# Kernel tuning notes

Measured on AMD Instinct MI355X. Metric: run time of the kernel, lower is better.

The kernel has to match this reference:

```python
import jax, jax.numpy as jnp
import numpy as np

D_MODEL = 1024
N_HEADS = 16
D_HEAD = D_MODEL // N_HEADS
SPARSE_THRESH = 0.09
MASK_FILL = -1e9


def setup_inputs() -> dict:
    key = jax.random.key(0)
    ks = jax.random.split(key, 11)
    B, S, D = 4, 1024, D_MODEL
    # Xavier-uniform bound for square [D, D] linear weights
    bound = float(np.sqrt(6.0 / (D + D)))

    def xavier(k):
        return jax.random.uniform(k, (D, D), jnp.float32, -bound, bound)

    return {
        "q": jax.random.normal(ks[0], (B, S, D), jnp.float32),
        "k": jax.random.normal(ks[1], (B, S, D), jnp.float32),
        "v": jax.random.normal(ks[2], (B, S, D), jnp.float32),
        "Wq": xavier(ks[3]), "bq": jnp.zeros((D,), jnp.float32),
        "Wk": xavier(ks[4]), "bk": jnp.zeros((D,), jnp.float32),
        "Wv": xavier(ks[5]), "bv": jnp.zeros((D,), jnp.float32),
        "Wo": xavier(ks[6]), "bo": jnp.zeros((D,), jnp.float32),
    }


def reference(q, k, v, Wq, bq, Wk, bk, Wv, bv, Wo, bo):
    B, S, D = q.shape
    H, dk = N_HEADS, D_HEAD

    def proj(x, W, b):
        # nn.Linear: x @ W^T + b, then split heads -> [B, H, S, dk]
        y = jnp.einsum("bsd,ed->bse", x, W) + b
        return y.reshape(B, S, H, dk).transpose(0, 2, 1, 3)

    qh = proj(q, Wq, bq)
    kh = proj(k, Wk, bk)
    vh = proj(v, Wv, bv)

    scale = 1.0 / jnp.sqrt(jnp.asarray(dk, q.dtype))
    scores = jnp.einsum("bhqd,bhkd->bhqk", qh, kh) * scale  # [B,H,S,S]

    att1 = jax.nn.softmax(scores, axis=-1)
    # mask entries whose first-pass probability is below the sparsity threshold
    scores2 = jnp.where(att1 < SPARSE_THRESH, jnp.asarray(MASK_FILL, scores.dtype), scores)
    att2 = jax.nn.softmax(scores2, axis=-1)
    # dropout(p=0.2) is identity in eval mode (deterministic reference)

    ctx = jnp.einsum("bhqk,bhkd->bhqd", att2, vh)           # [B,H,S,dk]
    ctx = ctx.transpose(0, 2, 1, 3).reshape(B, S, D)
    return jnp.einsum("bsd,ed->bse", ctx, Wo) + bo
```

## Files before the change

kernel.cpp:

```cpp
#include <hip/hip_runtime.h>
#include <hip/hip_bf16.h>
#include <math.h>


constexpr int D_MODEL = 1024;
constexpr int N_HEADS = 16;
constexpr int D_HEAD  = 64;
constexpr int SEQ     = 1024;
constexpr int BATCH   = 4;
constexpr float SPARSE_THRESH = 0.09f;

typedef short  bf16x8 __attribute__((ext_vector_type(8)));
typedef float  f32x4  __attribute__((ext_vector_type(4)));

__device__ __forceinline__ unsigned short f2bf_rne(float x) {
    unsigned u = __float_as_uint(x);
    u += 0x7FFFu + ((u >> 16) & 1u);
    return (unsigned short)(u >> 16);
}
__device__ __forceinline__ float bf2f(unsigned short b) {
    return __uint_as_float(((unsigned)b) << 16);
}

__device__ __forceinline__ unsigned cvt2(float a, float b) {
    __hip_bfloat162 p = __float22bfloat162_rn(make_float2(a, b));
    unsigned u; __builtin_memcpy(&u, &p, 4); return u;
}
__device__ __forceinline__ void split4(float x0, float x1, float x2, float x3,
                                       unsigned* hw, unsigned* lw) {
    const unsigned uh0 = cvt2(x0, x1);
    hw[0] = uh0;
    lw[0] = cvt2(x0 - __uint_as_float(uh0 << 16),
                 x1 - __uint_as_float(uh0 & 0xFFFF0000u));
    const unsigned uh1 = cvt2(x2, x3);
    hw[1] = uh1;
    lw[1] = cvt2(x2 - __uint_as_float(uh1 << 16),
                 x3 - __uint_as_float(uh1 & 0xFFFF0000u));
}

union BF8 { unsigned u[4]; bf16x8 v; };

__device__ __forceinline__ void unpack_pair(const unsigned* u, bf16x8& hi, bf16x8& lo) {
    BF8 h, l;
    #pragma unroll
    for (int p = 0; p < 4; ++p) {
        h.u[p] = (u[2 * p] >> 16)      | (u[2 * p + 1] & 0xFFFF0000u);
        l.u[p] = (u[2 * p] & 0xFFFFu)  | (u[2 * p + 1] << 16);
    }
    hi = h.v; lo = l.v;
}

__global__ __launch_bounds__(256)
void conv_w(const float* __restrict__ Wq, const float* __restrict__ Wk,
            const float* __restrict__ Wv,
            unsigned short* __restrict__ Wqh, unsigned short* __restrict__ Wql,
            unsigned short* __restrict__ Wkh, unsigned short* __restrict__ Wkl,
            unsigned short* __restrict__ Wvh, unsigned short* __restrict__ Wvl)
{
    const int NW8 = (D_MODEL * D_MODEL) / 8;
    int i = blockIdx.x * 256 + threadIdx.x;
    const float* s; unsigned short *dh, *dl;
    if (i < NW8)            { s = Wq; dh = Wqh; dl = Wql; }
    else if (i < 2 * NW8)   { i -= NW8; s = Wk; dh = Wkh; dl = Wkl; }
    else                    { i -= 2 * NW8; s = Wv; dh = Wvh; dl = Wvl; }
    const float4 x0 = ((const float4*)(s + (size_t)i * 8))[0];
    const float4 x1 = ((const float4*)(s + (size_t)i * 8))[1];
    unsigned hw[4], lw[4];
    split4(x0.x, x0.y, x0.z, x0.w, &hw[0], &lw[0]);
    split4(x1.x, x1.y, x1.z, x1.w, &hw[2], &lw[2]);
    *(uint4*)&dh[(size_t)i * 8] = *(const uint4*)hw;
    *(uint4*)&dl[(size_t)i * 8] = *(const uint4*)lw;
}

__global__ __launch_bounds__(256, 3)
void proj_qkv(const float* __restrict__ q, const float* __restrict__ k,
              const float* __restrict__ v,
              const unsigned short* __restrict__ Wqh, const unsigned short* __restrict__ Wql,
              const unsigned short* __restrict__ Wkh, const unsigned short* __restrict__ Wkl,
              const unsigned short* __restrict__ Wvh, const unsigned short* __restrict__ Wvl,
              const float* __restrict__ bq, const float* __restrict__ bk,
              const float* __restrict__ bv,
              unsigned* __restrict__ qp, unsigned* __restrict__ kp,
              unsigned short* __restrict__ vt)
{
    __shared__ unsigned short SM[4][128][40];
    unsigned short (*A_h)[40] = SM[0];
    unsigned short (*A_l)[40] = SM[1];
    unsigned short (*B_h)[40] = SM[2];
    unsigned short (*B_l)[40] = SM[3];

    const int z = blockIdx.z;
    const float* X    = (z == 0) ? q   : (z == 1) ? k   : v;
    const unsigned short* Wh = (z == 0) ? Wqh : (z == 1) ? Wkh : Wvh;
    const unsigned short* Wl = (z == 0) ? Wql : (z == 1) ? Wkl : Wvl;
    const float* bias = (z == 0) ? bq  : (z == 1) ? bk  : bv;
    const float scale = (z == 0) ? 0.125f : 1.0f;

    const int K = D_MODEL;
    const int tid = threadIdx.x, lane = tid & 63;
    const int l15 = lane & 15, l4 = lane >> 4;
    const int wv4 = tid >> 6;
    const int wr = (wv4 >> 1) * 64, wc = (wv4 & 1) * 64;
    const int bm = blockIdx.x * 128, bn = blockIdx.y * 128;
    const int sr = tid >> 1, sh = (tid & 1) * 16;

    f32x4 acc[4][4];
    #pragma unroll
    for (int i = 0; i < 4; ++i)
        #pragma unroll
        for (int j = 0; j < 4; ++j) acc[i][j] = (f32x4){0.f, 0.f, 0.f, 0.f};

    const float* ga = X + (size_t)(bm + sr) * K + sh;
    const unsigned short* gbh = Wh + (size_t)(bn + sr) * K + sh;
    const unsigned short* gbl = Wl + (size_t)(bn + sr) * K + sh;

    float4 av[4];
    uint4 wbh0, wbh1, wbl0, wbl1;
    #pragma unroll
    for (int l = 0; l < 4; ++l) av[l] = *(const float4*)&ga[l * 4];
    wbh0 = *(const uint4*)&gbh[0]; wbh1 = *(const uint4*)&gbh[8];
    wbl0 = *(const uint4*)&gbl[0]; wbl1 = *(const uint4*)&gbl[8];

    #pragma unroll 1
    for (int k0 = 0; k0 < K; k0 += 32) {
        unsigned ahw[8], alw[8];
        #pragma unroll
        for (int l = 0; l < 4; ++l)
            split4(av[l].x, av[l].y, av[l].z, av[l].w, &ahw[l * 2], &alw[l * 2]);

        __syncthreads();
        *(uint4*)&A_h[sr][sh]     = *(const uint4*)&ahw[0];
        *(uint4*)&A_h[sr][sh + 8] = *(const uint4*)&ahw[4];
        *(uint4*)&A_l[sr][sh]     = *(const uint4*)&alw[0];
        *(uint4*)&A_l[sr][sh + 8] = *(const uint4*)&alw[4];
        *(uint4*)&B_h[sr][sh]     = wbh0;
        *(uint4*)&B_h[sr][sh + 8] = wbh1;
        *(uint4*)&B_l[sr][sh]     = wbl0;
        *(uint4*)&B_l[sr][sh + 8] = wbl1;
        __syncthreads();

        if (k0 + 32 < K) {
            const int o = k0 + 32;
            #pragma unroll
            for (int l = 0; l < 4; ++l) av[l] = *(const float4*)&ga[o + l * 4];
            wbh0 = *(const uint4*)&gbh[o]; wbh1 = *(const uint4*)&gbh[o + 8];
            wbl0 = *(const uint4*)&gbl[o]; wbl1 = *(const uint4*)&gbl[o + 8];
        }

        bf16x8 ah[4], al4[4], bh4[4], bl4[4];
        #pragma unroll
        for (int i = 0; i < 4; ++i) {
            const int r = wr + i * 16 + l15;
            const int c = wc + i * 16 + l15;
            ah[i]  = *(const bf16x8*)&A_h[r][l4 * 8];
            al4[i] = *(const bf16x8*)&A_l[r][l4 * 8];
            bh4[i] = *(const bf16x8*)&B_h[c][l4 * 8];
            bl4[i] = *(const bf16x8*)&B_l[c][l4 * 8];
        }
        #pragma unroll
        for (int i = 0; i < 4; ++i)
            #pragma unroll
            for (int j = 0; j < 4; ++j) {
                acc[i][j] = __builtin_amdgcn_mfma_f32_16x16x32_bf16(ah[i],  bh4[j], acc[i][j], 0, 0, 0);
                acc[i][j] = __builtin_amdgcn_mfma_f32_16x16x32_bf16(ah[i],  bl4[j], acc[i][j], 0, 0, 0);
                acc[i][j] = __builtin_amdgcn_mfma_f32_16x16x32_bf16(al4[i], bh4[j], acc[i][j], 0, 0, 0);
            }
    }

    if (z == 2) {
        unsigned short* T = &SM[0][0][0];
        __syncthreads();
        #pragma unroll
        for (int i = 0; i < 4; ++i)
            #pragma unroll
            for (int j = 0; j < 4; ++j) {
                const int cl = wc + j * 16 + l15;
                const int sl = wr + i * 16 + l4 * 4;
                const float bi = bias[bn + cl];
                unsigned short h4[4];
                #pragma unroll
                for (int r = 0; r < 4; ++r)
                    h4[r] = f2bf_rne(acc[i][j][r] + bi);
                *(uint2*)&T[cl * 136 + sl] = *(const uint2*)&h4[0];
            }
        __syncthreads();
        const int c = tid >> 1, half = tid & 1;
        const int bb = bm >> 10;
        const int sb = (bm & (SEQ - 1)) + half * 64;
        unsigned short* dst = vt + (((size_t)bb << 20) + (size_t)(bn + c) * SEQ + sb);
        const unsigned short* srcT = &T[c * 136 + half * 64];
        #pragma unroll
        for (int u = 0; u < 8; ++u)
            *(uint4*)&dst[u * 8] = *(const uint4*)&srcT[u * 8];
        return;
    }

    unsigned* Cp = (z == 0) ? qp : kp;
    #pragma unroll
    for (int i = 0; i < 4; ++i)
        #pragma unroll
        for (int j = 0; j < 4; ++j) {
            const int rb = bm + wr + i * 16 + l4 * 4;
            const int c  = bn + wc + j * 16 + l15;
            const float bi = bias[c];
            const int h = c >> 6, d = c & (D_HEAD - 1);
            #pragma unroll
            for (int r = 0; r < 4; ++r) {
                const float val = (acc[i][j][r] + bi) * scale;
                const unsigned short hu = f2bf_rne(val);
                const unsigned short lu = f2bf_rne(val - bf2f(hu));
                const int mrow = rb + r;
                const int b = mrow >> 10, s = mrow & (SEQ - 1);
                Cp[((size_t)(b * N_HEADS + h) * SEQ + s) * D_HEAD + d] =
                    ((unsigned)hu << 16) | lu;
            }
        }
}

__global__ __launch_bounds__(256, 3)
void proj_o(const unsigned short* __restrict__ Act, const float* __restrict__ W,
            const float* __restrict__ bias, float* __restrict__ out)
{
    __shared__ unsigned short A_h[128][40];
    __shared__ unsigned short B_h[128][40];

    const int K = D_MODEL;
    const int tid = threadIdx.x, lane = tid & 63;
    const int l15 = lane & 15, l4 = lane >> 4;
    const int wv4 = tid >> 6;
    const int wr = (wv4 >> 1) * 64, wc = (wv4 & 1) * 64;
    const int bm = blockIdx.x * 128, bn = blockIdx.y * 128;
    const int sr = tid >> 1, sh = (tid & 1) * 16;

    f32x4 acc[4][4];
    #pragma unroll
    for (int i = 0; i < 4; ++i)
        #pragma unroll
        for (int j = 0; j < 4; ++j) acc[i][j] = (f32x4){0.f, 0.f, 0.f, 0.f};

    const unsigned short* ga = Act + (size_t)(bm + sr) * K + sh;
    const float* gb = W + (size_t)(bn + sr) * K + sh;

    uint4 av0 = *(const uint4*)&ga[0], av1 = *(const uint4*)&ga[8];
    float4 bv4[4];
    #pragma unroll
    for (int l = 0; l < 4; ++l) bv4[l] = *(const float4*)&gb[l * 4];

    #pragma unroll 1
    for (int k0 = 0; k0 < K; k0 += 32) {
        unsigned bhw[8];
        #pragma unroll
        for (int l = 0; l < 4; ++l) {
            bhw[l * 2]     = cvt2(bv4[l].x, bv4[l].y);
            bhw[l * 2 + 1] = cvt2(bv4[l].z, bv4[l].w);
        }

        __syncthreads();
        *(uint4*)&A_h[sr][sh]     = av0;
        *(uint4*)&A_h[sr][sh + 8] = av1;
        *(uint4*)&B_h[sr][sh]     = *(const uint4*)&bhw[0];
        *(uint4*)&B_h[sr][sh + 8] = *(const uint4*)&bhw[4];
        __syncthreads();

        if (k0 + 32 < K) {
            av0 = *(const uint4*)&ga[k0 + 32];
            av1 = *(const uint4*)&ga[k0 + 32 + 8];
            #pragma unroll
            for (int l = 0; l < 4; ++l)
                bv4[l] = *(const float4*)&gb[k0 + 32 + l * 4];
        }

        bf16x8 ah[4], bh4[4];
        #pragma unroll
        for (int i = 0; i < 4; ++i) {
            ah[i]  = *(const bf16x8*)&A_h[wr + i * 16 + l15][l4 * 8];
            bh4[i] = *(const bf16x8*)&B_h[wc + i * 16 + l15][l4 * 8];
        }
        #pragma unroll
        for (int i = 0; i < 4; ++i)
            #pragma unroll
            for (int j = 0; j < 4; ++j)
                acc[i][j] = __builtin_amdgcn_mfma_f32_16x16x32_bf16(ah[i], bh4[j], acc[i][j], 0, 0, 0);
    }

    #pragma unroll
    for (int i = 0; i < 4; ++i)
        #pragma unroll
        for (int j = 0; j < 4; ++j) {
            const int rb = bm + wr + i * 16 + l4 * 4;
            const int c  = bn + wc + j * 16 + l15;
            const float bi = bias[c];
            #pragma unroll
            for (int r = 0; r < 4; ++r)
                out[(size_t)(rb + r) * D_MODEL + c] = acc[i][j][r] + bi;
        }
}

__device__ __forceinline__ void score_from_lds(
    const unsigned short (* __restrict__ KH)[72], const unsigned short (* __restrict__ KL)[72],
    int l15, int l4, const bf16x8 (&qh)[2][2], const bf16x8 (&ql)[2][2], f32x4 acc[2][4])
{
    #pragma unroll
    for (int j = 0; j < 4; ++j) {
        const int row = l15 + 16 * j;
        const bf16x8 kh0 = *(const bf16x8*)&KH[row][l4 * 8];
        const bf16x8 kh1 = *(const bf16x8*)&KH[row][32 + l4 * 8];
        const bf16x8 kl0 = *(const bf16x8*)&KL[row][l4 * 8];
        const bf16x8 kl1 = *(const bf16x8*)&KL[row][32 + l4 * 8];
        #pragma unroll
        for (int st = 0; st < 2; ++st) {
            f32x4 a = (f32x4){0.f, 0.f, 0.f, 0.f};
            a = __builtin_amdgcn_mfma_f32_16x16x32_bf16(qh[st][0], kh0, a, 0, 0, 0);
            a = __builtin_amdgcn_mfma_f32_16x16x32_bf16(qh[st][0], kl0, a, 0, 0, 0);
            a = __builtin_amdgcn_mfma_f32_16x16x32_bf16(ql[st][0], kh0, a, 0, 0, 0);
            a = __builtin_amdgcn_mfma_f32_16x16x32_bf16(qh[st][1], kh1, a, 0, 0, 0);
            a = __builtin_amdgcn_mfma_f32_16x16x32_bf16(qh[st][1], kl1, a, 0, 0, 0);
            a = __builtin_amdgcn_mfma_f32_16x16x32_bf16(ql[st][1], kh1, a, 0, 0, 0);
            acc[st][j] = a;
        }
    }
}

__global__ __launch_bounds__(256, 3)
void attn_mfma(const unsigned* __restrict__ qp, const unsigned* __restrict__ kp,
               const unsigned short* __restrict__ vt, unsigned short* __restrict__ ctxh)
{
    __shared__ unsigned short KHL[2][2][64][72];
    __shared__ unsigned short Wl[4][32][64];
    __shared__ float Vm[64];
    __shared__ int AnyNU;
    float (*Pm)[4] = (float (*)[4])&Wl[0][0][0];

    const int tid  = threadIdx.x;
    const int lane = tid & 63;
    const int wv   = tid >> 6;
    const int l15  = lane & 15, l4 = lane >> 4;
    const int bh   = blockIdx.x;
    const int b    = bh >> 4, h = bh & 15;
    const int q0   = blockIdx.y * 128 + wv * 32;

    bf16x8 qh[2][2], ql[2][2];
    #pragma unroll
    for (int st = 0; st < 2; ++st) {
        const unsigned* qrow = qp + ((size_t)bh * SEQ + q0 + st * 16 + l15) * D_HEAD;
        #pragma unroll
        for (int ks = 0; ks < 2; ++ks) {
            unsigned u[8];
            *(uint4*)&u[0] = *(const uint4*)&qrow[ks * 32 + l4 * 8];
            *(uint4*)&u[4] = *(const uint4*)&qrow[ks * 32 + l4 * 8 + 4];
            unpack_pair(u, qh[st][ks], ql[st][ks]);
        }
    }

    const unsigned short* vtb = vt + (size_t)bh * D_HEAD * SEQ;

    {
        const int d = tid >> 2, q4 = tid & 3;
        const unsigned short* vr = vtb + (size_t)d * SEQ + q4 * 256;
        float s0 = 0.f, s1 = 0.f, s2 = 0.f, s3 = 0.f;
        #pragma unroll 4
        for (int i = 0; i < 32; ++i) {
            bf16x8 v8 = *(const bf16x8*)&vr[i * 8];
            s0 += bf2f((unsigned short)v8[0]) + bf2f((unsigned short)v8[4]);
            s1 += bf2f((unsigned short)v8[1]) + bf2f((unsigned short)v8[5]);
            s2 += bf2f((unsigned short)v8[2]) + bf2f((unsigned short)v8[6]);
            s3 += bf2f((unsigned short)v8[3]) + bf2f((unsigned short)v8[7]);
        }
        Pm[d][q4] = (s0 + s1) + (s2 + s3);
        if (tid == 0) AnyNU = 0;
    }

    const int sr = tid >> 2;
    const int sd = (tid & 3) * 16;
    const unsigned* kpb = kp + (size_t)bh * SEQ * D_HEAD;

    {
        unsigned u[16];
        const unsigned* src = kpb + (size_t)sr * D_HEAD + sd;
        #pragma unroll
        for (int g = 0; g < 4; ++g) *(uint4*)&u[g * 4] = *(const uint4*)&src[g * 4];
        bf16x8 h0, l0, h1, l1;
        unpack_pair(&u[0], h0, l0);
        unpack_pair(&u[8], h1, l1);
        *(bf16x8*)&KHL[0][0][sr][sd]     = h0;
        *(bf16x8*)&KHL[0][0][sr][sd + 8] = h1;
        *(bf16x8*)&KHL[0][1][sr][sd]     = l0;
        *(bf16x8*)&KHL[0][1][sr][sd + 8] = l1;
    }
    __syncthreads();

    float vm_local;
    if (tid < 64)
        vm_local = (Pm[tid][0] + Pm[tid][1] + Pm[tid][2] + Pm[tid][3]) * (1.f / 1024.f);
    if (tid < 64) Vm[tid] = vm_local;

    float mloc[2][4], zloc[2][4];
    #pragma unroll
    for (int st = 0; st < 2; ++st)
        #pragma unroll
        for (int r = 0; r < 4; ++r) { mloc[st][r] = -1e30f; zloc[st][r] = 0.f; }

    int cur = 0;

    #pragma unroll 1
    for (int c = 0; c < 16; ++c) {
        unsigned u[16];
        const int cn = (c + 1) & 15;
        const unsigned* src = kpb + ((size_t)cn * 64 + sr) * D_HEAD + sd;
        #pragma unroll
        for (int g = 0; g < 4; ++g) *(uint4*)&u[g * 4] = *(const uint4*)&src[g * 4];

        f32x4 acc[2][4];
        score_from_lds(KHL[cur][0], KHL[cur][1], l15, l4, qh, ql, acc);

        #pragma unroll
        for (int st = 0; st < 2; ++st)
            #pragma unroll
            for (int r = 0; r < 4; ++r) {
                const float a0 = acc[st][0][r], a1 = acc[st][1][r];
                const float a2 = acc[st][2][r], a3 = acc[st][3][r];
                mloc[st][r] = fmaxf(mloc[st][r], fmaxf(fmaxf(a0, a1), fmaxf(a2, a3)));
                zloc[st][r] += (__expf(a0) + __expf(a1)) + (__expf(a2) + __expf(a3));
            }

        bf16x8 h0, l0, h1, l1;
        unpack_pair(&u[0], h0, l0);
        unpack_pair(&u[8], h1, l1);
        const int nxt = cur ^ 1;
        *(bf16x8*)&KHL[nxt][0][sr][sd]     = h0;
        *(bf16x8*)&KHL[nxt][0][sr][sd + 8] = h1;
        *(bf16x8*)&KHL[nxt][1][sr][sd]     = l0;
        *(bf16x8*)&KHL[nxt][1][sr][sd + 8] = l1;
        __syncthreads();
        cur = nxt;
    }

    float taue[2][4];
    bool  unif[2][4];
    int mynu = 0;
    #pragma unroll
    for (int st = 0; st < 2; ++st)
        #pragma unroll
        for (int r = 0; r < 4; ++r) {
            float mm = mloc[st][r], zz = zloc[st][r];
            #pragma unroll
            for (int o = 1; o <= 8; o <<= 1) {
                mm = fmaxf(mm, __shfl_xor(mm, o, 16));
                zz += __shfl_xor(zz, o, 16);
            }
            const float tau = __logf(SPARSE_THRESH * zz);
            const bool uni = (mm < tau);
            unif[st][r] = uni;
            taue[st][r] = uni ? 3.0e38f : tau;
            mynu |= uni ? 0 : 1;
        }
    if (__any(mynu)) { if (lane == 0) atomicOr(&AnyNU, 1); }
    __syncthreads();
    const bool runB = (AnyNU != 0);

    float z2[2][4];
    f32x4 pv[2][4];
    #pragma unroll
    for (int st = 0; st < 2; ++st)
        #pragma unroll
        for (int r = 0; r < 4; ++r) { z2[st][r] = 0.f; pv[st][r] = (f32x4){0.f, 0.f, 0.f, 0.f}; }

    if (runB) {
        #pragma unroll 1
        for (int c = 0; c < 16; ++c) {
            unsigned u[16];
            const int cn = (c + 1) & 15;
            const unsigned* src = kpb + ((size_t)cn * 64 + sr) * D_HEAD + sd;
            #pragma unroll
            for (int g = 0; g < 4; ++g) *(uint4*)&u[g * 4] = *(const uint4*)&src[g * 4];

            f32x4 acc[2][4];
            score_from_lds(KHL[cur][0], KHL[cur][1], l15, l4, qh, ql, acc);

            int any = 0;
            #pragma unroll
            for (int st = 0; st < 2; ++st)
                #pragma unroll
                for (int r = 0; r < 4; ++r) {
                    const float rmax = fmaxf(fmaxf(acc[st][0][r], acc[st][1][r]),
                                             fmaxf(acc[st][2][r], acc[st][3][r]));
                    any |= (rmax >= taue[st][r]) ? 1 : 0;
                }

            if (__any(any)) {
                #pragma unroll
                for (int st = 0; st < 2; ++st)
                    #pragma unroll
                    for (int j = 0; j < 4; ++j)
                        #pragma unroll
                        for (int r = 0; r < 4; ++r) {
                            const float a = acc[st][j][r];
                            const float w = (a >= taue[st][r]) ? __expf(a) : 0.f;
                            const unsigned short wb = f2bf_rne(w);
                            z2[st][r] += bf2f(wb);
                            Wl[wv][st * 16 + l4 * 4 + r][l15 + 16 * j] = wb;
                        }
                asm volatile("s_waitcnt lgkmcnt(0)" ::: "memory");
                __builtin_amdgcn_sched_barrier(0);

                bf16x8 wa[2][2];
                #pragma unroll
                for (int st = 0; st < 2; ++st)
                    #pragma unroll
                    for (int ks = 0; ks < 2; ++ks)
                        wa[st][ks] = *(const bf16x8*)&Wl[wv][st * 16 + l15][ks * 32 + l4 * 8];

                #pragma unroll
                for (int ds = 0; ds < 4; ++ds) {
                    const bf16x8 v0 = *(const bf16x8*)
                        &vtb[(size_t)(ds * 16 + l15) * SEQ + c * 64 + l4 * 8];
                    const bf16x8 v1 = *(const bf16x8*)
                        &vtb[(size_t)(ds * 16 + l15) * SEQ + c * 64 + 32 + l4 * 8];
                    #pragma unroll
                    for (int st = 0; st < 2; ++st) {
                        pv[st][ds] = __builtin_amdgcn_mfma_f32_16x16x32_bf16(wa[st][0], v0, pv[st][ds], 0, 0, 0);
                        pv[st][ds] = __builtin_amdgcn_mfma_f32_16x16x32_bf16(wa[st][1], v1, pv[st][ds], 0, 0, 0);
                    }
                }
            }

            bf16x8 h0, l0, h1, l1;
            unpack_pair(&u[0], h0, l0);
            unpack_pair(&u[8], h1, l1);
            const int nxt = cur ^ 1;
            *(bf16x8*)&KHL[nxt][0][sr][sd]     = h0;
            *(bf16x8*)&KHL[nxt][0][sr][sd + 8] = h1;
            *(bf16x8*)&KHL[nxt][1][sr][sd]     = l0;
            *(bf16x8*)&KHL[nxt][1][sr][sd + 8] = l1;
            __syncthreads();
            cur = nxt;
        }

        #pragma unroll
        for (int st = 0; st < 2; ++st)
            #pragma unroll
            for (int r = 0; r < 4; ++r) {
                #pragma unroll
                for (int o = 1; o <= 8; o <<= 1) z2[st][r] += __shfl_xor(z2[st][r], o, 16);
            }
    }

    float* Tw = (float*)&KHL[0][0][0][0] + wv * 2176;
    #pragma unroll
    for (int st = 0; st < 2; ++st)
        #pragma unroll
        for (int r = 0; r < 4; ++r) {
            const float inv = unif[st][r] ? 0.f : (1.f / z2[st][r]);
            const int row = st * 16 + l4 * 4 + r;
            #pragma unroll
            for (int ds = 0; ds < 4; ++ds) {
                const int d = ds * 16 + l15;
                Tw[row * 68 + d] = unif[st][r] ? Vm[d] : pv[st][ds][r] * inv;
            }
        }
    asm volatile("s_waitcnt lgkmcnt(0)" ::: "memory");
    __builtin_amdgcn_sched_barrier(0);

    const int rr = lane >> 1, seg = lane & 1;
    const size_t gbase = ((size_t)b * SEQ + q0 + rr) * D_MODEL + h * D_HEAD + seg * 32;
    #pragma unroll
    for (int u2 = 0; u2 < 8; ++u2) {
        const float4 t = *(const float4*)&Tw[rr * 68 + seg * 32 + u2 * 4];
        unsigned short h4[4] = {f2bf_rne(t.x), f2bf_rne(t.y), f2bf_rne(t.z), f2bf_rne(t.w)};
        *(uint2*)&ctxh[gbase + u2 * 4] = *(const uint2*)h4;
    }
}

extern "C" void kernel_launch(void* const* d_in, const int* in_sizes, int n_in,
                              void* d_out, int out_size, void* d_ws, size_t ws_size,
                              hipStream_t stream)
{
    const float* q  = (const float*)d_in[0];
    const float* k  = (const float*)d_in[1];
    const float* v  = (const float*)d_in[2];
    const float* Wq = (const float*)d_in[3];
    const float* bq = (const float*)d_in[4];
    const float* Wk = (const float*)d_in[5];
    const float* bk = (const float*)d_in[6];
    const float* Wv = (const float*)d_in[7];
    const float* bv = (const float*)d_in[8];
    const float* Wo = (const float*)d_in[9];
    const float* bo = (const float*)d_in[10];
    float* out = (float*)d_out;

    const size_t MB = 1 << 20;
    char* w = (char*)d_ws;
    unsigned* qp = (unsigned*)(w);
    unsigned* kp = (unsigned*)(w + 16 * MB);
    unsigned short* vt   = (unsigned short*)(w + 32 * MB);
    unsigned short* ctxh = (unsigned short*)(w + 40 * MB);
    unsigned short* Wqh = (unsigned short*)(w + 48 * MB);
    unsigned short* Wql = (unsigned short*)(w + 50 * MB);
    unsigned short* Wkh = (unsigned short*)(w + 52 * MB);
    unsigned short* Wkl = (unsigned short*)(w + 54 * MB);
    unsigned short* Wvh = (unsigned short*)(w + 56 * MB);
    unsigned short* Wvl = (unsigned short*)(w + 58 * MB);

    const int NW8 = (D_MODEL * D_MODEL) / 8;

    conv_w<<<(3 * NW8) / 256, 256, 0, stream>>>(Wq, Wk, Wv, Wqh, Wql, Wkh, Wkl, Wvh, Wvl);

    proj_qkv<<<dim3(32, 8, 3), 256, 0, stream>>>(q, k, v,
                                                 Wqh, Wql, Wkh, Wkl, Wvh, Wvl,
                                                 bq, bk, bv, qp, kp, vt);

    attn_mfma<<<dim3(BATCH * N_HEADS, SEQ / 128), 256, 0, stream>>>(qp, kp, vt, ctxh);

    proj_o<<<dim3(32, 8), 256, 0, stream>>>(ctxh, Wo, bo, out);
}
```

Measured before the change: 178.6 us.

## Store K as pre-swizzled hi/lo planes and stream via global_load_lds

New measurement: 179.2 us. About the same (+0.4%).

```diff
diff --git a/kernel.cpp b/kernel.cpp
--- a/kernel.cpp
+++ b/kernel.cpp
@@ -48,6 +48,12 @@
         l.u[p] = (u[2 * p] & 0xFFFFu)  | (u[2 * p + 1] << 16);
     }
     hi = h.v; lo = l.v;
+}
+
+__device__ __forceinline__ void gld_lds16(const void* g, void* l) {
+    __builtin_amdgcn_global_load_lds(
+        (const __attribute__((address_space(1))) void*)g,
+        (__attribute__((address_space(3))) void*)l, 16, 0, 0);
 }
 
 __global__ __launch_bounds__(256)
@@ -80,7 +86,8 @@
               const unsigned short* __restrict__ Wvh, const unsigned short* __restrict__ Wvl,
               const float* __restrict__ bq, const float* __restrict__ bk,
               const float* __restrict__ bv,
-              unsigned* __restrict__ qp, unsigned* __restrict__ kp,
+              unsigned* __restrict__ qp,
+              unsigned short* __restrict__ khh, unsigned short* __restrict__ khl,
               unsigned short* __restrict__ vt)
 {
     __shared__ unsigned short SM[4][128][40];
@@ -94,7 +101,6 @@
     const unsigned short* Wh = (z == 0) ? Wqh : (z == 1) ? Wkh : Wvh;
     const unsigned short* Wl = (z == 0) ? Wql : (z == 1) ? Wkl : Wvl;
     const float* bias = (z == 0) ? bq  : (z == 1) ? bk  : bv;
-    const float scale = (z == 0) ? 0.125f : 1.0f;
 
     const int K = D_MODEL;
     const int tid = threadIdx.x, lane = tid & 63;
@@ -195,26 +201,49 @@
         return;
     }
 
-    unsigned* Cp = (z == 0) ? qp : kp;
-    #pragma unroll
-    for (int i = 0; i < 4; ++i)
-        #pragma unroll
-        for (int j = 0; j < 4; ++j) {
-            const int rb = bm + wr + i * 16 + l4 * 4;
-            const int c  = bn + wc + j * 16 + l15;
-            const float bi = bias[c];
-            const int h = c >> 6, d = c & (D_HEAD - 1);
-            #pragma unroll
-            for (int r = 0; r < 4; ++r) {
-                const float val = (acc[i][j][r] + bi) * scale;
-                const unsigned short hu = f2bf_rne(val);
-                const unsigned short lu = f2bf_rne(val - bf2f(hu));
-                const int mrow = rb + r;
-                const int b = mrow >> 10, s = mrow & (SEQ - 1);
-                Cp[((size_t)(b * N_HEADS + h) * SEQ + s) * D_HEAD + d] =
-                    ((unsigned)hu << 16) | lu;
-            }
-        }
+    if (z == 0) {
+        #pragma unroll
+        for (int i = 0; i < 4; ++i)
+            #pragma unroll
+            for (int j = 0; j < 4; ++j) {
+                const int rb = bm + wr + i * 16 + l4 * 4;
+                const int c  = bn + wc + j * 16 + l15;
+                const float bi = bias[c];
+                const int h = c >> 6, d = c & (D_HEAD - 1);
+                #pragma unroll
+                for (int r = 0; r < 4; ++r) {
+                    const float val = (acc[i][j][r] + bi) * 0.125f;
+                    const unsigned short hu = f2bf_rne(val);
+                    const unsigned short lu = f2bf_rne(val - bf2f(hu));
+                    const int mrow = rb + r;
+                    const int b = mrow >> 10, s = mrow & (SEQ - 1);
+                    qp[((size_t)(b * N_HEADS + h) * SEQ + s) * D_HEAD + d] =
+                        ((unsigned)hu << 16) | lu;
+                }
+            }
+    } else {
+        #pragma unroll
+        for (int i = 0; i < 4; ++i)
+            #pragma unroll
+            for (int j = 0; j < 4; ++j) {
+                const int rb = bm + wr + i * 16 + l4 * 4;
+                const int c  = bn + wc + j * 16 + l15;
+                const float bi = bias[c];
+                const int h = c >> 6, d = c & (D_HEAD - 1);
+                #pragma unroll
+                for (int r = 0; r < 4; ++r) {
+                    const float val = acc[i][j][r] + bi;
+                    const unsigned short hu = f2bf_rne(val);
+                    const unsigned short lu = f2bf_rne(val - bf2f(hu));
+                    const int mrow = rb + r;
+                    const int b = mrow >> 10, s = mrow & (SEQ - 1);
+                    const int dsw = d ^ ((s & 7) << 3);
+                    const size_t off = ((size_t)(b * N_HEADS + h) * SEQ + s) * D_HEAD + dsw;
+                    khh[off] = hu;
+                    khl[off] = lu;
+                }
+            }
+    }
 }
 
 __global__ __launch_bounds__(256, 3)
@@ -297,16 +326,17 @@
 }
 
 __device__ __forceinline__ void score_from_lds(
-    const unsigned short (* __restrict__ KH)[72], const unsigned short (* __restrict__ KL)[72],
-    int l15, int l4, const bf16x8 (&qh)[2][2], const bf16x8 (&ql)[2][2], f32x4 acc[2][4])
+    const unsigned short (* __restrict__ KH)[64], const unsigned short (* __restrict__ KL)[64],
+    int l15, int dk0, int dk1,
+    const bf16x8 (&qh)[2][2], const bf16x8 (&ql)[2][2], f32x4 acc[2][4])
 {
     #pragma unroll
     for (int j = 0; j < 4; ++j) {
         const int row = l15 + 16 * j;
-        const bf16x8 kh0 = *(const bf16x8*)&KH[row][l4 * 8];
-        const bf16x8 kh1 = *(const bf16x8*)&KH[row][32 + l4 * 8];
-        const bf16x8 kl0 = *(const bf16x8*)&KL[row][l4 * 8];
-        const bf16x8 kl1 = *(const bf16x8*)&KL[row][32 + l4 * 8];
+        const bf16x8 kh0 = *(const bf16x8*)&KH[row][dk0];
+        const bf16x8 kh1 = *(const bf16x8*)&KH[row][dk1];
+        const bf16x8 kl0 = *(const bf16x8*)&KL[row][dk0];
+        const bf16x8 kl1 = *(const bf16x8*)&KL[row][dk1];
         #pragma unroll
         for (int st = 0; st < 2; ++st) {
             f32x4 a = (f32x4){0.f, 0.f, 0.f, 0.f};
@@ -322,10 +352,11 @@
 }
 
 __global__ __launch_bounds__(256, 3)
-void attn_mfma(const unsigned* __restrict__ qp, const unsigned* __restrict__ kp,
+void attn_mfma(const unsigned* __restrict__ qp,
+               const unsigned short* __restrict__ khh, const unsigned short* __restrict__ khl,
                const unsigned short* __restrict__ vt, unsigned short* __restrict__ ctxh)
 {
-    __shared__ unsigned short KHL[2][2][64][72];
+    __shared__ unsigned short KHL[2][2][64][64];
     __shared__ unsigned short Wl[4][32][64];
     __shared__ float Vm[64];
     __shared__ int AnyNU;
@@ -338,6 +369,10 @@
     const int bh   = blockIdx.x;
     const int b    = bh >> 4, h = bh & 15;
     const int q0   = blockIdx.y * 128 + wv * 32;
+
+    const int swz = (l15 & 7) << 3;
+    const int dk0 = (l4 * 8) ^ swz;
+    const int dk1 = (32 + l4 * 8) ^ swz;
 
     bf16x8 qh[2][2], ql[2][2];
     #pragma unroll
@@ -370,29 +405,20 @@
         if (tid == 0) AnyNU = 0;
     }
 
-    const int sr = tid >> 2;
-    const int sd = (tid & 3) * 16;
-    const unsigned* kpb = kp + (size_t)bh * SEQ * D_HEAD;
-
-    {
-        unsigned u[16];
-        const unsigned* src = kpb + (size_t)sr * D_HEAD + sd;
-        #pragma unroll
-        for (int g = 0; g < 4; ++g) *(uint4*)&u[g * 4] = *(const uint4*)&src[g * 4];
-        bf16x8 h0, l0, h1, l1;
-        unpack_pair(&u[0], h0, l0);
-        unpack_pair(&u[8], h1, l1);
-        *(bf16x8*)&KHL[0][0][sr][sd]     = h0;
-        *(bf16x8*)&KHL[0][0][sr][sd + 8] = h1;
-        *(bf16x8*)&KHL[0][1][sr][sd]     = l0;
-        *(bf16x8*)&KHL[0][1][sr][sd + 8] = l1;
+    const size_t kbase = (size_t)bh * SEQ * D_HEAD;
+    const int krow0 = wv * 16 + (lane >> 3);
+    const int dgrp  = (lane & 7) * 8;
+
+    #pragma unroll
+    for (int t = 0; t < 2; ++t) {
+        const size_t src = kbase + (size_t)(krow0 + t * 8) * D_HEAD + dgrp;
+        gld_lds16(khh + src, &KHL[0][0][wv * 16 + t * 8][0]);
+        gld_lds16(khl + src, &KHL[0][1][wv * 16 + t * 8][0]);
     }
     __syncthreads();
 
-    float vm_local;
     if (tid < 64)
-        vm_local = (Pm[tid][0] + Pm[tid][1] + Pm[tid][2] + Pm[tid][3]) * (1.f / 1024.f);
-    if (tid < 64) Vm[tid] = vm_local;
+        Vm[tid] = (Pm[tid][0] + Pm[tid][1] + Pm[tid][2] + Pm[tid][3]) * (1.f / 1024.f);
 
     float mloc[2][4], zloc[2][4];
     #pragma unroll
@@ -404,14 +430,17 @@
 
     #pragma unroll 1
     for (int c = 0; c < 16; ++c) {
-        unsigned u[16];
         const int cn = (c + 1) & 15;
-        const unsigned* src = kpb + ((size_t)cn * 64 + sr) * D_HEAD + sd;
-        #pragma unroll
-        for (int g = 0; g < 4; ++g) *(uint4*)&u[g * 4] = *(const uint4*)&src[g * 4];
+        const int nxt = cur ^ 1;
+        #pragma unroll
+        for (int t = 0; t < 2; ++t) {
+            const size_t src = kbase + ((size_t)cn * 64 + krow0 + t * 8) * D_HEAD + dgrp;
+            gld_lds16(khh + src, &KHL[nxt][0][wv * 16 + t * 8][0]);
+            gld_lds16(khl + src, &KHL[nxt][1][wv * 16 + t * 8][0]);
+        }
 
         f32x4 acc[2][4];
-        score_from_lds(KHL[cur][0], KHL[cur][1], l15, l4, qh, ql, acc);
+        score_from_lds(KHL[cur][0], KHL[cur][1], l15, dk0, dk1, qh, ql, acc);
 
         #pragma unroll
         for (int st = 0; st < 2; ++st)
@@ -423,14 +452,6 @@
                 zloc[st][r] += (__expf(a0) + __expf(a1)) + (__expf(a2) + __expf(a3));
             }
 
-        bf16x8 h0, l0, h1, l1;
-        unpack_pair(&u[0], h0, l0);
-        unpack_pair(&u[8], h1, l1);
-        const int nxt = cur ^ 1;
-        *(bf16x8*)&KHL[nxt][0][sr][sd]     = h0;
-        *(bf16x8*)&KHL[nxt][0][sr][sd + 8] = h1;
-        *(bf16x8*)&KHL[nxt][1][sr][sd]     = l0;
-        *(bf16x8*)&KHL[nxt][1][sr][sd + 8] = l1;
         __syncthreads();
         cur = nxt;
     }
@@ -468,14 +489,17 @@
     if (runB) {
         #pragma unroll 1
         for (int c = 0; c < 16; ++c) {
-            unsigned u[16];
             const int cn = (c + 1) & 15;
-            const unsigned* src = kpb + ((size_t)cn * 64 + sr) * D_HEAD + sd;
-            #pragma unroll
-            for (int g = 0; g < 4; ++g) *(uint4*)&u[g * 4] = *(const uint4*)&src[g * 4];
+            const int nxt = cur ^ 1;
+            #pragma unroll
+            for (int t = 0; t < 2; ++t) {
+                const size_t src = kbase + ((size_t)cn * 64 + krow0 + t * 8) * D_HEAD + dgrp;
+                gld_lds16(khh + src, &KHL[nxt][0][wv * 16 + t * 8][0]);
+                gld_lds16(khl + src, &KHL[nxt][1][wv * 16 + t * 8][0]);
+            }
 
             f32x4 acc[2][4];
-            score_from_lds(KHL[cur][0], KHL[cur][1], l15, l4, qh, ql, acc);
+            score_from_lds(KHL[cur][0], KHL[cur][1], l15, dk0, dk1, qh, ql, acc);
 
             int any = 0;
             #pragma unroll
@@ -524,14 +548,6 @@
                 }
             }
 
-            bf16x8 h0, l0, h1, l1;
-            unpack_pair(&u[0], h0, l0);
-            unpack_pair(&u[8], h1, l1);
-            const int nxt = cur ^ 1;
-            *(bf16x8*)&KHL[nxt][0][sr][sd]     = h0;
-            *(bf16x8*)&KHL[nxt][0][sr][sd + 8] = h1;
-            *(bf16x8*)&KHL[nxt][1][sr][sd]     = l0;
-            *(bf16x8*)&KHL[nxt][1][sr][sd + 8] = l1;
             __syncthreads();
             cur = nxt;
         }
@@ -545,7 +561,8 @@
             }
     }
 
-    float* Tw = (float*)&KHL[0][0][0][0] + wv * 2176;
+    float* Tw = (float*)&KHL[0][0][0][0] + wv * 2048;
+    __syncthreads();
     #pragma unroll
     for (int st = 0; st < 2; ++st)
         #pragma unroll
@@ -555,7 +572,7 @@
             #pragma unroll
             for (int ds = 0; ds < 4; ++ds) {
                 const int d = ds * 16 + l15;
-                Tw[row * 68 + d] = unif[st][r] ? Vm[d] : pv[st][ds][r] * inv;
+                Tw[row * 64 + d] = unif[st][r] ? Vm[d] : pv[st][ds][r] * inv;
             }
         }
     asm volatile("s_waitcnt lgkmcnt(0)" ::: "memory");
@@ -565,7 +582,7 @@
     const size_t gbase = ((size_t)b * SEQ + q0 + rr) * D_MODEL + h * D_HEAD + seg * 32;
     #pragma unroll
     for (int u2 = 0; u2 < 8; ++u2) {
-        const float4 t = *(const float4*)&Tw[rr * 68 + seg * 32 + u2 * 4];
+        const float4 t = *(const float4*)&Tw[rr * 64 + seg * 32 + u2 * 4];
         unsigned short h4[4] = {f2bf_rne(t.x), f2bf_rne(t.y), f2bf_rne(t.z), f2bf_rne(t.w)};
         *(uint2*)&ctxh[gbase + u2 * 4] = *(const uint2*)h4;
     }
@@ -591,7 +608,8 @@
     const size_t MB = 1 << 20;
     char* w = (char*)d_ws;
     unsigned* qp = (unsigned*)(w);
-    unsigned* kp = (unsigned*)(w + 16 * MB);
+    unsigned short* khh  = (unsigned short*)(w + 16 * MB);
+    unsigned short* khl  = (unsigned short*)(w + 24 * MB);
     unsigned short* vt   = (unsigned short*)(w + 32 * MB);
     unsigned short* ctxh = (unsigned short*)(w + 40 * MB);
     unsigned short* Wqh = (unsigned short*)(w + 48 * MB);
@@ -607,9 +625,9 @@
 
     proj_qkv<<<dim3(32, 8, 3), 256, 0, stream>>>(q, k, v,
                                                  Wqh, Wql, Wkh, Wkl, Wvh, Wvl,
-                                                 bq, bk, bv, qp, kp, vt);
-
-    attn_mfma<<<dim3(BATCH * N_HEADS, SEQ / 128), 256, 0, stream>>>(qp, kp, vt, ctxh);
+                                                 bq, bk, bv, qp, khh, khl, vt);
+
+    attn_mfma<<<dim3(BATCH * N_HEADS, SEQ / 128), 256, 0, stream>>>(qp, khh, khl, vt, ctxh);
 
     proj_o<<<dim3(32, 8), 256, 0, stream>>>(ctxh, Wo, bo, out);
 }
```
